# Kernel optimization log

Hardware: AMD Instinct MI355X
Metric: run time of the kernel (lower is better)

## Reference

```python
import jax, jax.numpy as jnp
import numpy as np

H = 128  # LSTM units per direction


def _lstm_last_state(x_proj, Wr, b):
    """x_proj: [T,B,4H] precomputed input projection. Returns final hidden [B,H]."""
    B = x_proj.shape[1]
    h0 = jnp.zeros((B, H), x_proj.dtype)
    c0 = jnp.zeros((B, H), x_proj.dtype)

    def step(carry, xt):
        h, c = carry
        z = xt + h @ Wr + b  # [B,4H]
        i, f, g, o = jnp.split(z, 4, axis=-1)  # keras gate order: i, f, c(g), o
        i = jax.nn.sigmoid(i)
        f = jax.nn.sigmoid(f)
        g = jnp.tanh(g)
        o = jax.nn.sigmoid(o)
        c = f * c + i * g
        h = o * jnp.tanh(c)
        return (h, c), None

    (h, c), _ = jax.lax.scan(step, (h0, c0), x_proj)
    return h


def setup_inputs() -> dict:
    key = jax.random.key(0)
    ks = jax.random.split(key, 8)
    B, T, D = 128, 256, 1024
    s_in = 1.0 / np.sqrt(D)
    s_rec = 1.0 / np.sqrt(H)
    return {
        "x": jax.random.normal(ks[0], (B, T, D), jnp.float32),  # precomputed ELMo embeddings
        "Wf_k": jax.random.normal(ks[1], (D, 4 * H), jnp.float32) * s_in,
        "Wf_r": jax.random.normal(ks[2], (H, 4 * H), jnp.float32) * s_rec,
        "bf": jnp.zeros((4 * H,), jnp.float32),
        "Wb_k": jax.random.normal(ks[3], (D, 4 * H), jnp.float32) * s_in,
        "Wb_r": jax.random.normal(ks[4], (H, 4 * H), jnp.float32) * s_rec,
        "bb": jnp.zeros((4 * H,), jnp.float32),
        "W1": jax.random.normal(ks[5], (2 * H, 32), jnp.float32) * (1.0 / np.sqrt(2 * H)),
        "b1": jnp.zeros((32,), jnp.float32),
        "W2": jax.random.normal(ks[6], (32, 2), jnp.float32) * (1.0 / np.sqrt(32)),
        "b2": jnp.zeros((2,), jnp.float32),
    }


def reference(x, Wf_k, Wf_r, bf, Wb_k, Wb_r, bb, W1, b1, W2, b2):
    # Bidirectional LSTM over ELMo embeddings x: [B,T,D]; dropout inactive (inference).
    xp_f = jnp.einsum('btd,dg->tbg', x, Wf_k)            # [T,B,4H]
    h_fwd = _lstm_last_state(xp_f, Wf_r, bf)             # [B,H]
    xp_b = jnp.einsum('btd,dg->tbg', x[:, ::-1, :], Wb_k)
    h_bwd = _lstm_last_state(xp_b, Wb_r, bb)             # [B,H]
    h = jnp.concatenate([h_fwd, h_bwd], axis=-1)         # [B,2H]
    y = jax.nn.relu(h @ W1 + b1)                          # [B,32]
    return jax.nn.sigmoid(y @ W2 + b2)                    # [B,2]
```

## Files before the change

### kernel.cpp

```cpp
#include <hip/hip_runtime.h>
#include <cstdint>
#include <cstddef>


typedef __attribute__((ext_vector_type(8))) short short8;
typedef __attribute__((ext_vector_type(4))) float f32x4;
typedef __attribute__((address_space(1))) unsigned int gas_uint;
typedef __attribute__((address_space(3))) unsigned int las_uint;
typedef __attribute__((address_space(1))) const unsigned short as1_us;

__device__ __forceinline__ unsigned short f2b(float f) {
    unsigned int u = __float_as_uint(f);
    u += 0x7FFFu + ((u >> 16) & 1u);
    return (unsigned short)(u >> 16);
}
__device__ __forceinline__ float b2f(unsigned short u) {
    return __uint_as_float(((unsigned int)u) << 16);
}
__device__ __forceinline__ unsigned int cvt_pk_bf16(float a, float b) {
    unsigned int r;
    asm("v_cvt_pk_bf16_f32 %0, %1, %2" : "=v"(r) : "v"(a), "v"(b));
    return r;
}
__device__ __forceinline__ float rcp_(float x) { return __builtin_amdgcn_rcpf(x); }
__device__ __forceinline__ float sigmoidf_(float z) { return rcp_(1.0f + __expf(-z)); }
__device__ __forceinline__ float tanhf_(float z) {
    float e = __expf(2.0f * z);
    return 1.0f - 2.0f * rcp_(e + 1.0f);
}

#define LITE_BARRIER() asm volatile("s_waitcnt lgkmcnt(0)\n\ts_barrier" ::: "memory")

__device__ __forceinline__ void async_ld16(const unsigned short* g, unsigned short* l) {
    __builtin_amdgcn_global_load_lds(
        (gas_uint*)(uintptr_t)g,
        (las_uint*)(uintptr_t)(unsigned int)(uintptr_t)l,
        16, 0, 0);
}

__global__ void conv_wk(const float* __restrict__ wf, const float* __restrict__ wb,
                        unsigned short* __restrict__ wt) {
    int dir = blockIdx.y;
    const float* w = dir ? wb : wf;
    int id = blockIdx.x * blockDim.x + threadIdx.x;
    int g = id >> 10, d = id & 1023;
    wt[(size_t)dir * 524288 + id] = f2b(w[d * 512 + g]);
}

__global__ __launch_bounds__(256, 2) void gemm_xp(
    const float* __restrict__ X,
    const unsigned short* __restrict__ Wt,
    const float* __restrict__ bf_, const float* __restrict__ bb_,
    unsigned short* __restrict__ XP)
{
    __shared__ unsigned short As[128 * 64];
    __shared__ unsigned short Bs[256 * 64];

    const int tid  = threadIdx.x;

    const int flat = blockIdx.x + 256 * (blockIdx.y + 2 * blockIdx.z);
    const int xcd  = flat & 7;
    const int p    = flat >> 3;
    const int tnp  = p & 1;
    const int dir  = (p >> 1) & 1;
    const int tm   = xcd * 32 + (p >> 2);

    const int w    = tid >> 6;
    const int lane = tid & 63;
    const int lanelo = lane & 15;
    const int quad = lane >> 4;
    const int wm = w & 1, wn = w >> 1;

    const unsigned short* Bmat = Wt + (size_t)dir * 524288;
    const float* bias = dir ? bb_ : bf_;
    unsigned short* out = XP + (size_t)dir * 16777216;

    const float* gax[4];
    unsigned short* la[4];
    const unsigned short* gb[8];
    unsigned short* lb[8];
#pragma unroll
    for (int c = 0; c < 4; ++c) {
        int p2 = c * 256 + tid;
        int row = p2 >> 3;
        int lc = (p2 & 7) ^ (row & 7);
        gax[c] = X + (size_t)(tm * 128 + row) * 1024 + lc * 8;
        la[c]  = As + (size_t)p2 * 8;
    }
#pragma unroll
    for (int c = 0; c < 8; ++c) {
        int p2 = c * 256 + tid;
        int row = p2 >> 3;
        int lc = (p2 & 7) ^ (row & 7);
        gb[c] = Bmat + (size_t)(tnp * 256 + row) * 1024 + lc * 8;
        lb[c] = Bs + (size_t)(c * 256 + (tid & ~63)) * 8;
    }

    float4 xr[4][2];
#pragma unroll
    for (int c = 0; c < 4; ++c) {
        xr[c][0] = *(const float4*)(gax[c]);
        xr[c][1] = *(const float4*)(gax[c] + 4);
    }

    f32x4 acc[4][8];
#pragma unroll
    for (int i = 0; i < 4; i++)
#pragma unroll
        for (int j = 0; j < 8; j++) acc[i][j] = (f32x4){0.f, 0.f, 0.f, 0.f};

    for (int kt = 0; kt < 16; ++kt) {
        LITE_BARRIER();
#pragma unroll
        for (int c = 0; c < 4; ++c) {
            uint4 s;
            s.x = cvt_pk_bf16(xr[c][0].x, xr[c][0].y);
            s.y = cvt_pk_bf16(xr[c][0].z, xr[c][0].w);
            s.z = cvt_pk_bf16(xr[c][1].x, xr[c][1].y);
            s.w = cvt_pk_bf16(xr[c][1].z, xr[c][1].w);
            *(uint4*)la[c] = s;
        }
#pragma unroll
        for (int c = 0; c < 8; ++c) async_ld16(gb[c] + kt * 64, lb[c]);
        __builtin_amdgcn_sched_barrier(0);
        if (kt < 15) {
#pragma unroll
            for (int c = 0; c < 4; ++c) {
                xr[c][0] = *(const float4*)(gax[c] + (kt + 1) * 64);
                xr[c][1] = *(const float4*)(gax[c] + (kt + 1) * 64 + 4);
            }
            __builtin_amdgcn_sched_barrier(0);
            asm volatile("s_waitcnt vmcnt(8)" ::: "memory");
        } else {
            asm volatile("s_waitcnt vmcnt(0)" ::: "memory");
        }
        LITE_BARRIER();

#pragma unroll
        for (int ks = 0; ks < 2; ++ks) {
            short8 af[4], bfr[8];
#pragma unroll
            for (int i = 0; i < 4; ++i) {
                int row = wm * 64 + i * 16 + lanelo;
                af[i] = *(const short8*)(As + row * 64 + (((ks * 4 + quad) ^ (row & 7)) * 8));
            }
#pragma unroll
            for (int j = 0; j < 8; ++j) {
                int row = wn * 128 + j * 16 + lanelo;
                bfr[j] = *(const short8*)(Bs + row * 64 + (((ks * 4 + quad) ^ (row & 7)) * 8));
            }
#pragma unroll
            for (int i = 0; i < 4; ++i)
#pragma unroll
                for (int j = 0; j < 8; ++j)
                    acc[i][j] = __builtin_amdgcn_mfma_f32_16x16x32_bf16(af[i], bfr[j], acc[i][j], 0, 0, 0);
        }
    }

    float biasv[8];
#pragma unroll
    for (int j = 0; j < 8; ++j)
        biasv[j] = bias[tnp * 256 + wn * 128 + j * 16 + lanelo];

#pragma unroll
    for (int i = 0; i < 4; ++i) {
#pragma unroll
        for (int r = 0; r < 4; ++r) {
            int gr = tm * 128 + wm * 64 + i * 16 + quad * 4 + r;
            int bb = gr >> 8, tt = gr & 255;
            size_t orow = (size_t)(tt * 128 + bb) * 512;
#pragma unroll
            for (int j = 0; j < 8; ++j) {
                int col = tnp * 256 + wn * 128 + j * 16 + lanelo;
                out[orow + col] = f2b(acc[i][j][r] + biasv[j]);
            }
        }
    }
}

__global__ __launch_bounds__(512, 2) void lstm_rec(
    const unsigned short* __restrict__ XP,
    const float* __restrict__ Wfr, const float* __restrict__ Wbr,
    float* __restrict__ Hout)
{
    __shared__ unsigned short h_lds[2][128];

    const int tid    = threadIdx.x;
    const int w      = tid >> 6;
    const int lane   = tid & 63;
    const int lanelo = lane & 15;
    const int quad   = lane >> 4;
    const int dir    = blockIdx.x >> 7;
    const int seq    = blockIdx.x & 127;
    const int dim    = w * 16 + lanelo;

    const float* Wr = dir ? Wbr : Wfr;
    const unsigned short* xp = XP + (size_t)dir * 16777216;

    short8 wrf[4][4];
#pragma unroll
    for (int g = 0; g < 4; ++g)
#pragma unroll
        for (int ks = 0; ks < 4; ++ks) {
            short8 f;
#pragma unroll
            for (int j = 0; j < 8; ++j)
                f[j] = (short)f2b(Wr[(size_t)(ks * 32 + quad * 8 + j) * 512 + g * 128 + dim]);
            wrf[g][ks] = f;
        }

    if (tid < 128) ((unsigned short*)h_lds)[tid] = 0;

    short8 hfrag[4];
    const short8 hz = (short8){0, 0, 0, 0, 0, 0, 0, 0};
#pragma unroll
    for (int ks = 0; ks < 4; ++ks) hfrag[ks] = hz;

    float cv = 0.f, hv = 0.f;

    const ptrdiff_t xstep = dir ? -65536 : 65536;
    const unsigned short* xb_ =
        xp + (size_t)(dir ? 255 : 0) * 65536 + (size_t)seq * 512 + dim;

    unsigned int xA[4], xB[4], xC[4], xD[4];

#define XLOAD(BUF)                                                               \
    {                                                                            \
        const as1_us* xg = (const as1_us*)(uintptr_t)xb_;                        \
        _Pragma("unroll")                                                        \
        for (int g = 0; g < 4; ++g) BUF[g] = xg[g * 128];                        \
        xb_ += xstep;                                                            \
    }

    XLOAD(xA)
    XLOAD(xB)
    XLOAD(xC)
    XLOAD(xD)

    LITE_BARRIER();

    const f32x4 kZ = (f32x4){0.f, 0.f, 0.f, 0.f};

#define LSTM_STEP(XC_, CUR, NXT)                                                 \
    {                                                                            \
               \
        float xv0 = b2f((unsigned short)XC_[0]);                                 \
        float xv1 = b2f((unsigned short)XC_[1]);                                 \
        float xv2 = b2f((unsigned short)XC_[2]);                                 \
        float xv3 = b2f((unsigned short)XC_[3]);                                 \
        XLOAD(XC_)                                                               \
                                     \
        if (lanelo == 0) {                                                       \
            _Pragma("unroll")                                                    \
            for (int ks = 0; ks < 4; ++ks)                                       \
                hfrag[ks] = *(const short8*)(&h_lds[CUR][ks * 32 + quad * 8]);   \
        }                                                                        \
                               \
        f32x4 z0 = __builtin_amdgcn_mfma_f32_16x16x32_bf16(hfrag[0], wrf[0][0], kZ, 0, 0, 0); \
        f32x4 z1 = __builtin_amdgcn_mfma_f32_16x16x32_bf16(hfrag[0], wrf[1][0], kZ, 0, 0, 0); \
        f32x4 z2 = __builtin_amdgcn_mfma_f32_16x16x32_bf16(hfrag[0], wrf[2][0], kZ, 0, 0, 0); \
        f32x4 z3 = __builtin_amdgcn_mfma_f32_16x16x32_bf16(hfrag[0], wrf[3][0], kZ, 0, 0, 0); \
        _Pragma("unroll")                                                        \
        for (int ks = 1; ks < 4; ++ks) {                                         \
            z0 = __builtin_amdgcn_mfma_f32_16x16x32_bf16(hfrag[ks], wrf[0][ks], z0, 0, 0, 0); \
            z1 = __builtin_amdgcn_mfma_f32_16x16x32_bf16(hfrag[ks], wrf[1][ks], z1, 0, 0, 0); \
            z2 = __builtin_amdgcn_mfma_f32_16x16x32_bf16(hfrag[ks], wrf[2][ks], z2, 0, 0, 0); \
            z3 = __builtin_amdgcn_mfma_f32_16x16x32_bf16(hfrag[ks], wrf[3][ks], z3, 0, 0, 0); \
        }                                                                        \
                      \
        if (quad == 0) {                                                         \
            float zi = z0[0] + xv0, zf = z1[0] + xv1;                            \
            float zg = z2[0] + xv2, zo = z3[0] + xv3;                            \
            float iv = sigmoidf_(zi), fv = sigmoidf_(zf);                        \
            float gv = tanhf_(zg),    ov = sigmoidf_(zo);                        \
            cv = fv * cv + iv * gv;                                              \
            hv = ov * tanhf_(cv);                                                \
            h_lds[NXT][dim] = f2b(hv);                                           \
        }                                                                        \
        LITE_BARRIER();                                                          \
    }

    for (int t = 0; t < 256; t += 4) {
        LSTM_STEP(xA, 0, 1)
        LSTM_STEP(xB, 1, 0)
        LSTM_STEP(xC, 0, 1)
        LSTM_STEP(xD, 1, 0)
    }
#undef LSTM_STEP
#undef XLOAD

    if (quad == 0)
        Hout[(size_t)(dir * 128 + seq) * 128 + dim] = hv;
}

__global__ void mlp_head(const float* __restrict__ Hout,
                         const float* __restrict__ W1, const float* __restrict__ b1,
                         const float* __restrict__ W2, const float* __restrict__ b2,
                         float* __restrict__ out)
{
    __shared__ float y1[32];
    int b = blockIdx.x;
    int j = threadIdx.x;
    const float* hf = Hout + (size_t)b * 128;
    const float* hb = Hout + (size_t)(128 + b) * 128;
    if (j < 32) {
        float acc = b1[j];
        for (int k = 0; k < 128; ++k) acc += hf[k] * W1[k * 32 + j];
        for (int k = 0; k < 128; ++k) acc += hb[k] * W1[(128 + k) * 32 + j];
        y1[j] = fmaxf(acc, 0.0f);
    }
    __syncthreads();
    if (j < 2) {
        float z = b2[j];
        for (int k = 0; k < 32; ++k) z += y1[k] * W2[k * 2 + j];
        out[b * 2 + j] = 1.0f / (1.0f + __expf(-z));
    }
}

extern "C" void kernel_launch(void* const* d_in, const int* in_sizes, int n_in,
                              void* d_out, int out_size, void* d_ws, size_t ws_size,
                              hipStream_t stream) {
    const float* x    = (const float*)d_in[0];
    const float* Wf_k = (const float*)d_in[1];
    const float* Wf_r = (const float*)d_in[2];
    const float* bf   = (const float*)d_in[3];
    const float* Wb_k = (const float*)d_in[4];
    const float* Wb_r = (const float*)d_in[5];
    const float* bb   = (const float*)d_in[6];
    const float* W1   = (const float*)d_in[7];
    const float* b1   = (const float*)d_in[8];
    const float* W2   = (const float*)d_in[9];
    const float* b2   = (const float*)d_in[10];
    float* out = (float*)d_out;

    char* ws = (char*)d_ws;
    const size_t OFF_WT   = 0;
    const size_t OFF_HOUT = 2097152;
    const size_t OFF_XP   = OFF_HOUT + 131072;

    unsigned short* wt  = (unsigned short*)(ws + OFF_WT);
    float*          ho  = (float*)(ws + OFF_HOUT);
    unsigned short* xpb = (unsigned short*)(ws + OFF_XP);

    conv_wk<<<dim3(2048, 2), dim3(256), 0, stream>>>(Wf_k, Wb_k, wt);
    gemm_xp<<<dim3(256, 2, 2), dim3(256), 0, stream>>>(x, wt, bf, bb, xpb);
    lstm_rec<<<dim3(256), dim3(512), 0, stream>>>(xpb, Wf_r, Wb_r, ho);
    mlp_head<<<dim3(128), dim3(64), 0, stream>>>(ho, W1, b1, W2, b2, out);
}
```

Measured before the change: 399.6 us.

## Double-buffer LDS tiles in input-projection GEMM and widen block to 512 threads

The input-projection GEMM now keeps two LDS buffers for its A and B tiles, so the next k-tile is converted and loaded asynchronously while MFMAs run on the current one. Only one barrier remains per step. The block grows from 256 to 512 threads (8 waves), with each wave owning a 64x64 sub-tile instead of 64x128, which halves per-thread accumulator registers. In exchange, LDS use doubles to 96KB per block and occupancy drops to one block per CU, and the recurrent kernel is unchanged.

```diff
diff --git a/kernel.cpp b/kernel.cpp
--- a/kernel.cpp
+++ b/kernel.cpp
@@ -47,14 +47,14 @@
     wt[(size_t)dir * 524288 + id] = f2b(w[d * 512 + g]);
 }
 
-__global__ __launch_bounds__(256, 2) void gemm_xp(
+__global__ __launch_bounds__(512, 1) void gemm_xp(
     const float* __restrict__ X,
     const unsigned short* __restrict__ Wt,
     const float* __restrict__ bf_, const float* __restrict__ bb_,
     unsigned short* __restrict__ XP)
 {
-    __shared__ unsigned short As[128 * 64];
-    __shared__ unsigned short Bs[256 * 64];
+    __shared__ unsigned short As[2][128 * 64];
+    __shared__ unsigned short Bs[2][256 * 64];
 
     const int tid  = threadIdx.x;
 
@@ -75,92 +75,125 @@
     const float* bias = dir ? bb_ : bf_;
     unsigned short* out = XP + (size_t)dir * 16777216;
 
-    const float* gax[4];
-    unsigned short* la[4];
-    const unsigned short* gb[8];
-    unsigned short* lb[8];
+    const float* gax[2];
+    int la_off[2];
+#pragma unroll
+    for (int c = 0; c < 2; ++c) {
+        int s = c * 512 + tid;
+        int row = s >> 3;
+        int lc = (s & 7) ^ (row & 7);
+        gax[c]   = X + (size_t)(tm * 128 + row) * 1024 + lc * 8;
+        la_off[c] = s * 8;
+    }
+    const unsigned short* gb[4];
+    int lb_off[4];
 #pragma unroll
     for (int c = 0; c < 4; ++c) {
-        int p2 = c * 256 + tid;
-        int row = p2 >> 3;
-        int lc = (p2 & 7) ^ (row & 7);
-        gax[c] = X + (size_t)(tm * 128 + row) * 1024 + lc * 8;
-        la[c]  = As + (size_t)p2 * 8;
-    }
-#pragma unroll
-    for (int c = 0; c < 8; ++c) {
-        int p2 = c * 256 + tid;
-        int row = p2 >> 3;
-        int lc = (p2 & 7) ^ (row & 7);
-        gb[c] = Bmat + (size_t)(tnp * 256 + row) * 1024 + lc * 8;
-        lb[c] = Bs + (size_t)(c * 256 + (tid & ~63)) * 8;
-    }
-
-    float4 xr[4][2];
-#pragma unroll
-    for (int c = 0; c < 4; ++c) {
+        int s = c * 512 + tid;
+        int row = s >> 3;
+        int lc = (s & 7) ^ (row & 7);
+        gb[c]    = Bmat + (size_t)(tnp * 256 + row) * 1024 + lc * 8;
+        lb_off[c] = (c * 512 + (tid & ~63)) * 8;
+    }
+
+    f32x4 acc[4][4];
+#pragma unroll
+    for (int i = 0; i < 4; i++)
+#pragma unroll
+        for (int j = 0; j < 4; j++) acc[i][j] = (f32x4){0.f, 0.f, 0.f, 0.f};
+
+    float4 xr[2][2];
+
+#pragma unroll
+    for (int c = 0; c < 2; ++c) {
         xr[c][0] = *(const float4*)(gax[c]);
         xr[c][1] = *(const float4*)(gax[c] + 4);
     }
-
-    f32x4 acc[4][8];
-#pragma unroll
-    for (int i = 0; i < 4; i++)
-#pragma unroll
-        for (int j = 0; j < 8; j++) acc[i][j] = (f32x4){0.f, 0.f, 0.f, 0.f};
-
-    for (int kt = 0; kt < 16; ++kt) {
-        LITE_BARRIER();
-#pragma unroll
-        for (int c = 0; c < 4; ++c) {
-            uint4 s;
-            s.x = cvt_pk_bf16(xr[c][0].x, xr[c][0].y);
-            s.y = cvt_pk_bf16(xr[c][0].z, xr[c][0].w);
-            s.z = cvt_pk_bf16(xr[c][1].x, xr[c][1].y);
-            s.w = cvt_pk_bf16(xr[c][1].z, xr[c][1].w);
-            *(uint4*)la[c] = s;
-        }
-#pragma unroll
-        for (int c = 0; c < 8; ++c) async_ld16(gb[c] + kt * 64, lb[c]);
-        __builtin_amdgcn_sched_barrier(0);
-        if (kt < 15) {
-#pragma unroll
-            for (int c = 0; c < 4; ++c) {
-                xr[c][0] = *(const float4*)(gax[c] + (kt + 1) * 64);
-                xr[c][1] = *(const float4*)(gax[c] + (kt + 1) * 64 + 4);
-            }
-            __builtin_amdgcn_sched_barrier(0);
-            asm volatile("s_waitcnt vmcnt(8)" ::: "memory");
-        } else {
-            asm volatile("s_waitcnt vmcnt(0)" ::: "memory");
-        }
-        LITE_BARRIER();
-
-#pragma unroll
-        for (int ks = 0; ks < 2; ++ks) {
-            short8 af[4], bfr[8];
-#pragma unroll
-            for (int i = 0; i < 4; ++i) {
-                int row = wm * 64 + i * 16 + lanelo;
-                af[i] = *(const short8*)(As + row * 64 + (((ks * 4 + quad) ^ (row & 7)) * 8));
-            }
-#pragma unroll
-            for (int j = 0; j < 8; ++j) {
-                int row = wn * 128 + j * 16 + lanelo;
-                bfr[j] = *(const short8*)(Bs + row * 64 + (((ks * 4 + quad) ^ (row & 7)) * 8));
-            }
-#pragma unroll
-            for (int i = 0; i < 4; ++i)
-#pragma unroll
-                for (int j = 0; j < 8; ++j)
-                    acc[i][j] = __builtin_amdgcn_mfma_f32_16x16x32_bf16(af[i], bfr[j], acc[i][j], 0, 0, 0);
-        }
-    }
-
-    float biasv[8];
-#pragma unroll
-    for (int j = 0; j < 8; ++j)
-        biasv[j] = bias[tnp * 256 + wn * 128 + j * 16 + lanelo];
+#pragma unroll
+    for (int c = 0; c < 2; ++c) {
+        uint4 s;
+        s.x = cvt_pk_bf16(xr[c][0].x, xr[c][0].y);
+        s.y = cvt_pk_bf16(xr[c][0].z, xr[c][0].w);
+        s.z = cvt_pk_bf16(xr[c][1].x, xr[c][1].y);
+        s.w = cvt_pk_bf16(xr[c][1].z, xr[c][1].w);
+        *(uint4*)(&As[0][la_off[c]]) = s;
+    }
+#pragma unroll
+    for (int c = 0; c < 4; ++c) async_ld16(gb[c], &Bs[0][lb_off[c]]);
+    __builtin_amdgcn_sched_barrier(0);
+#pragma unroll
+    for (int c = 0; c < 2; ++c) {
+        xr[c][0] = *(const float4*)(gax[c] + 64);
+        xr[c][1] = *(const float4*)(gax[c] + 64 + 4);
+    }
+    __builtin_amdgcn_sched_barrier(0);
+    asm volatile("s_waitcnt vmcnt(4)" ::: "memory");
+    LITE_BARRIER();
+
+#define GSTEP(CUR, NXT, KT)                                                      \
+    {                                                                            \
+        if ((KT) < 15) {                                                         \
+                        \
+            _Pragma("unroll")                                                    \
+            for (int c = 0; c < 2; ++c) {                                        \
+                uint4 s;                                                         \
+                s.x = cvt_pk_bf16(xr[c][0].x, xr[c][0].y);                       \
+                s.y = cvt_pk_bf16(xr[c][0].z, xr[c][0].w);                       \
+                s.z = cvt_pk_bf16(xr[c][1].x, xr[c][1].y);                       \
+                s.w = cvt_pk_bf16(xr[c][1].z, xr[c][1].w);                       \
+                *(uint4*)(&As[NXT][la_off[c]]) = s;                              \
+            }                                                                    \
+                                                  \
+            _Pragma("unroll")                                                    \
+            for (int c = 0; c < 4; ++c)                                          \
+                async_ld16(gb[c] + ((KT) + 1) * 64, &Bs[NXT][lb_off[c]]);        \
+            __builtin_amdgcn_sched_barrier(0);                                   \
+            if ((KT) < 14) {                                                     \
+                        \
+                _Pragma("unroll")                                                \
+                for (int c = 0; c < 2; ++c) {                                    \
+                    xr[c][0] = *(const float4*)(gax[c] + ((KT) + 2) * 64);       \
+                    xr[c][1] = *(const float4*)(gax[c] + ((KT) + 2) * 64 + 4);   \
+                }                                                                \
+                __builtin_amdgcn_sched_barrier(0);                               \
+            }                                                                    \
+        }                                                                        \
+                                                    \
+        _Pragma("unroll")                                                        \
+        for (int ks = 0; ks < 2; ++ks) {                                         \
+            short8 af[4], bfr[4];                                                \
+            _Pragma("unroll")                                                    \
+            for (int i = 0; i < 4; ++i) {                                        \
+                int row = wm * 64 + i * 16 + lanelo;                             \
+                af[i] = *(const short8*)(&As[CUR][row * 64 + (((ks * 4 + quad) ^ (row & 7)) * 8)]); \
+            }                                                                    \
+            _Pragma("unroll")                                                    \
+            for (int j = 0; j < 4; ++j) {                                        \
+                int row = wn * 64 + j * 16 + lanelo;                             \
+                bfr[j] = *(const short8*)(&Bs[CUR][row * 64 + (((ks * 4 + quad) ^ (row & 7)) * 8)]); \
+            }                                                                    \
+            _Pragma("unroll")                                                    \
+            for (int i = 0; i < 4; ++i)                                          \
+                _Pragma("unroll")                                                \
+                for (int j = 0; j < 4; ++j)                                      \
+                    acc[i][j] = __builtin_amdgcn_mfma_f32_16x16x32_bf16(af[i], bfr[j], acc[i][j], 0, 0, 0); \
+        }                                                                        \
+                  \
+        if ((KT) < 14)       asm volatile("s_waitcnt vmcnt(4)" ::: "memory");    \
+        else if ((KT) == 14) asm volatile("s_waitcnt vmcnt(0)" ::: "memory");    \
+        if ((KT) < 15) LITE_BARRIER();                                           \
+    }
+
+    for (int t = 0; t < 16; t += 2) {
+        GSTEP(0, 1, t)
+        GSTEP(1, 0, t + 1)
+    }
+#undef GSTEP
+
+    float biasv[4];
+#pragma unroll
+    for (int j = 0; j < 4; ++j)
+        biasv[j] = bias[tnp * 256 + wn * 64 + j * 16 + lanelo];
 
 #pragma unroll
     for (int i = 0; i < 4; ++i) {
@@ -170,8 +203,8 @@
             int bb = gr >> 8, tt = gr & 255;
             size_t orow = (size_t)(tt * 128 + bb) * 512;
 #pragma unroll
-            for (int j = 0; j < 8; ++j) {
-                int col = tnp * 256 + wn * 128 + j * 16 + lanelo;
+            for (int j = 0; j < 4; ++j) {
+                int col = tnp * 256 + wn * 64 + j * 16 + lanelo;
                 out[orow + col] = f2b(acc[i][j][r] + biasv[j]);
             }
         }
@@ -343,7 +376,7 @@
     unsigned short* xpb = (unsigned short*)(ws + OFF_XP);
 
     conv_wk<<<dim3(2048, 2), dim3(256), 0, stream>>>(Wf_k, Wb_k, wt);
-    gemm_xp<<<dim3(256, 2, 2), dim3(256), 0, stream>>>(x, wt, bf, bb, xpb);
+    gemm_xp<<<dim3(256, 2, 2), dim3(512), 0, stream>>>(x, wt, bf, bb, xpb);
     lstm_rec<<<dim3(256), dim3(512), 0, stream>>>(xpb, Wf_r, Wb_r, ho);
     mlp_head<<<dim3(128), dim3(64), 0, stream>>>(ho, W1, b1, W2, b2, out);
 }
```

New measurement: 432.2 us. 1.08x slower.

## Double-buffer B tile in LDS to prefetch next K-slice during MFMA

Applied to the files above, without the earlier changes.

The weight (B) tile in the input-projection GEMM now uses two LDS buffers. The async global-to-LDS load for step kt+1 is issued before computing step kt, and the wait allows 16 loads in flight instead of 8. The goal is to hide B-load latency behind MFMA work rather than stalling each iteration. In exchange, LDS use per block rises from 48KB to 80KB, which may cut occupancy below the requested 2 blocks per CU. The A tile is still single-buffered, and the barriers move to the end of each step.

```diff
diff --git a/kernel.cpp b/kernel.cpp
--- a/kernel.cpp
+++ b/kernel.cpp
@@ -54,7 +54,7 @@
     unsigned short* __restrict__ XP)
 {
     __shared__ unsigned short As[128 * 64];
-    __shared__ unsigned short Bs[256 * 64];
+    __shared__ unsigned short Bs[2][256 * 64];
 
     const int tid  = threadIdx.x;
 
@@ -78,7 +78,7 @@
     const float* gax[4];
     unsigned short* la[4];
     const unsigned short* gb[8];
-    unsigned short* lb[8];
+    int lb_off[8];
 #pragma unroll
     for (int c = 0; c < 4; ++c) {
         int p2 = c * 256 + tid;
@@ -92,8 +92,8 @@
         int p2 = c * 256 + tid;
         int row = p2 >> 3;
         int lc = (p2 & 7) ^ (row & 7);
-        gb[c] = Bmat + (size_t)(tnp * 256 + row) * 1024 + lc * 8;
-        lb[c] = Bs + (size_t)(c * 256 + (tid & ~63)) * 8;
+        gb[c]    = Bmat + (size_t)(tnp * 256 + row) * 1024 + lc * 8;
+        lb_off[c] = (c * 256 + (tid & ~63)) * 8;
     }
 
     float4 xr[4][2];
@@ -102,6 +102,10 @@
         xr[c][0] = *(const float4*)(gax[c]);
         xr[c][1] = *(const float4*)(gax[c] + 4);
     }
+    __builtin_amdgcn_sched_barrier(0);
+#pragma unroll
+    for (int c = 0; c < 8; ++c) async_ld16(gb[c], &Bs[0][lb_off[c]]);
+    __builtin_amdgcn_sched_barrier(0);
 
     f32x4 acc[4][8];
 #pragma unroll
@@ -109,53 +113,61 @@
 #pragma unroll
         for (int j = 0; j < 8; j++) acc[i][j] = (f32x4){0.f, 0.f, 0.f, 0.f};
 
-    for (int kt = 0; kt < 16; ++kt) {
-        LITE_BARRIER();
-#pragma unroll
-        for (int c = 0; c < 4; ++c) {
-            uint4 s;
-            s.x = cvt_pk_bf16(xr[c][0].x, xr[c][0].y);
-            s.y = cvt_pk_bf16(xr[c][0].z, xr[c][0].w);
-            s.z = cvt_pk_bf16(xr[c][1].x, xr[c][1].y);
-            s.w = cvt_pk_bf16(xr[c][1].z, xr[c][1].w);
-            *(uint4*)la[c] = s;
-        }
-#pragma unroll
-        for (int c = 0; c < 8; ++c) async_ld16(gb[c] + kt * 64, lb[c]);
-        __builtin_amdgcn_sched_barrier(0);
-        if (kt < 15) {
-#pragma unroll
-            for (int c = 0; c < 4; ++c) {
-                xr[c][0] = *(const float4*)(gax[c] + (kt + 1) * 64);
-                xr[c][1] = *(const float4*)(gax[c] + (kt + 1) * 64 + 4);
-            }
-            __builtin_amdgcn_sched_barrier(0);
-            asm volatile("s_waitcnt vmcnt(8)" ::: "memory");
-        } else {
-            asm volatile("s_waitcnt vmcnt(0)" ::: "memory");
-        }
-        LITE_BARRIER();
-
-#pragma unroll
-        for (int ks = 0; ks < 2; ++ks) {
-            short8 af[4], bfr[8];
-#pragma unroll
-            for (int i = 0; i < 4; ++i) {
-                int row = wm * 64 + i * 16 + lanelo;
-                af[i] = *(const short8*)(As + row * 64 + (((ks * 4 + quad) ^ (row & 7)) * 8));
-            }
-#pragma unroll
-            for (int j = 0; j < 8; ++j) {
-                int row = wn * 128 + j * 16 + lanelo;
-                bfr[j] = *(const short8*)(Bs + row * 64 + (((ks * 4 + quad) ^ (row & 7)) * 8));
-            }
-#pragma unroll
-            for (int i = 0; i < 4; ++i)
-#pragma unroll
-                for (int j = 0; j < 8; ++j)
-                    acc[i][j] = __builtin_amdgcn_mfma_f32_16x16x32_bf16(af[i], bfr[j], acc[i][j], 0, 0, 0);
-        }
-    }
+#define GSTEP(BCUR, BNXT, KT)                                                    \
+    {                                                                            \
+        _Pragma("unroll")                                                        \
+        for (int c = 0; c < 4; ++c) {                                            \
+            uint4 s;                                                             \
+            s.x = cvt_pk_bf16(xr[c][0].x, xr[c][0].y);                           \
+            s.y = cvt_pk_bf16(xr[c][0].z, xr[c][0].w);                           \
+            s.z = cvt_pk_bf16(xr[c][1].x, xr[c][1].y);                           \
+            s.w = cvt_pk_bf16(xr[c][1].z, xr[c][1].w);                           \
+            *(uint4*)la[c] = s;                                                  \
+        }                                                                        \
+        __builtin_amdgcn_sched_barrier(0);                                       \
+        if ((KT) < 15) {                                                         \
+            _Pragma("unroll")                                                    \
+            for (int c = 0; c < 4; ++c) {                                        \
+                xr[c][0] = *(const float4*)(gax[c] + ((KT) + 1) * 64);           \
+                xr[c][1] = *(const float4*)(gax[c] + ((KT) + 1) * 64 + 4);       \
+            }                                                                    \
+            __builtin_amdgcn_sched_barrier(0);                                   \
+            _Pragma("unroll")                                                    \
+            for (int c = 0; c < 8; ++c)                                          \
+                async_ld16(gb[c] + ((KT) + 1) * 64, &Bs[BNXT][lb_off[c]]);       \
+            __builtin_amdgcn_sched_barrier(0);                                   \
+            asm volatile("s_waitcnt vmcnt(16)" ::: "memory");                    \
+        } else {                                                                 \
+            asm volatile("s_waitcnt vmcnt(0)" ::: "memory");                     \
+        }                                                                        \
+        LITE_BARRIER();                           \
+        _Pragma("unroll")                                                        \
+        for (int ks = 0; ks < 2; ++ks) {                                         \
+            short8 af[4], bfr[8];                                                \
+            _Pragma("unroll")                                                    \
+            for (int i = 0; i < 4; ++i) {                                        \
+                int row = wm * 64 + i * 16 + lanelo;                             \
+                af[i] = *(const short8*)(As + row * 64 + (((ks * 4 + quad) ^ (row & 7)) * 8)); \
+            }                                                                    \
+            _Pragma("unroll")                                                    \
+            for (int j = 0; j < 8; ++j) {                                        \
+                int row = wn * 128 + j * 16 + lanelo;                            \
+                bfr[j] = *(const short8*)(&Bs[BCUR][row * 64 + (((ks * 4 + quad) ^ (row & 7)) * 8)]); \
+            }                                                                    \
+            _Pragma("unroll")                                                    \
+            for (int i = 0; i < 4; ++i)                                          \
+                _Pragma("unroll")                                                \
+                for (int j = 0; j < 8; ++j)                                      \
+                    acc[i][j] = __builtin_amdgcn_mfma_f32_16x16x32_bf16(af[i], bfr[j], acc[i][j], 0, 0, 0); \
+        }                                                                        \
+        LITE_BARRIER();                              \
+    }
+
+    for (int t = 0; t < 16; t += 2) {
+        GSTEP(0, 1, t)
+        GSTEP(1, 0, t + 1)
+    }
+#undef GSTEP
 
     float biasv[8];
 #pragma unroll
```

After: 500.5 us. +25.3%, slower.
